# Optimization experiments

Hardware: AMD Instinct MI355X
Metric: run time of the kernel (lower is better)

Reference implementation:

```python
import jax, jax.numpy as jnp
import numpy as np

D = 1024
H = 16
DK = D // H


def setup_inputs() -> dict:
    key = jax.random.key(0)
    ks = jax.random.split(key, 10)
    B, S = 2, 2048
    scale = 1.0 / np.sqrt(D)
    inp = {
        "x": jax.random.normal(ks[0], (B, S, D), dtype=jnp.float32),
        "mask": jax.random.randint(ks[1], (B, S), 0, 2, dtype=jnp.int32),
        "wq": jax.random.normal(ks[2], (D, D), dtype=jnp.float32) * scale,
        "bq": jnp.zeros((D,), dtype=jnp.float32),
        "wk": jax.random.normal(ks[3], (D, D), dtype=jnp.float32) * scale,
        "bk": jnp.zeros((D,), dtype=jnp.float32),
        "wv": jax.random.normal(ks[4], (D, D), dtype=jnp.float32) * scale,
        "bv": jnp.zeros((D,), dtype=jnp.float32),
        "wo": jax.random.normal(ks[5], (D, D), dtype=jnp.float32) * scale,
        "bo": jnp.zeros((D,), dtype=jnp.float32),
    }
    return inp


def reference(x, mask, wq, bq, wk, bk, wv, bv, wo, bo):
    B, S, _ = x.shape
    # torch Linear: y = x @ W.T + b
    def proj(w, b):
        return (jnp.einsum("bsd,ed->bse", x, w) + b).reshape(B, S, H, DK).transpose(0, 2, 1, 3)  # (B,H,S,dk)

    q = proj(wq, bq)
    k = proj(wk, bk)
    v = proj(wv, bv)

    scores = jnp.einsum("bhqd,bhkd->bhqk", q, k) / jnp.sqrt(jnp.float32(DK))  # (B,H,S,S)
    # original: mask.unsqueeze(1).unsqueeze(3) -> (B,1,S,1), masks along the QUERY axis
    m = mask[:, None, :, None]  # (B,1,S,1)
    scores = jnp.where(m == 0, jnp.float32(-1e9), scores)
    attn = jax.nn.softmax(scores, axis=-1)
    ctx = jnp.einsum("bhqk,bhkd->bhqd", attn, v)  # (B,H,S,dk)
    concat = ctx.transpose(0, 2, 1, 3).reshape(B, S, D)
    return jnp.einsum("bsd,ed->bse", concat, wo) + bo
```

## Files before the change

### kernel.cpp

```cpp
#include <hip/hip_runtime.h>
#include <hip/hip_bf16.h>

#define SEQ 2048
#define DM  1024

typedef __attribute__((ext_vector_type(8))) _Float16 f16x8;
typedef __attribute__((ext_vector_type(4)))  float   f32x4;

#define EXP2F(x) __builtin_amdgcn_exp2f(x)

__device__ __forceinline__ ushort f2h(float x) {
    union { _Float16 h; ushort u; } c; c.h = (_Float16)x; return c.u;
}
__device__ __forceinline__ unsigned pk2h(float a, float b) {
    typedef __fp16 fp16v2 __attribute__((ext_vector_type(2)));
    union { fp16v2 h; unsigned u; } c;
    c.h = __builtin_amdgcn_cvt_pkrtz(a, b);
    return c.u;
}

__device__ __forceinline__ void gload16(const void* g, void* l) {
    __builtin_amdgcn_global_load_lds(
        (const __attribute__((address_space(1))) unsigned*)(uintptr_t)g,
        (__attribute__((address_space(3))) unsigned*)(uintptr_t)l, 16, 0, 0);
}

__global__ __launch_bounds__(256)
void cvt_all(const float* __restrict__ x,  const float* __restrict__ wq,
             const float* __restrict__ wk, const float* __restrict__ wv,
             const float* __restrict__ wo,
             ushort* __restrict__ xH, ushort* __restrict__ wH)
{
    const int NX4 = (2 * SEQ * DM) / 4;
    const int NW4 = (DM * DM) / 4;
    const int total = NX4 + 4 * NW4;
    for (int i = blockIdx.x * 256 + threadIdx.x; i < total; i += gridDim.x * 256) {
        float4 v; ushort4* dst;
        if (i < NX4) {
            v = ((const float4*)x)[i];
            dst = (ushort4*)xH + i;
        } else {
            const int j = i - NX4;
            const int wi = j >> 18;
            const int jo = j & (NW4 - 1);
            const float* ws_ = (wi == 0) ? wq : (wi == 1) ? wk : (wi == 2) ? wv : wo;
            v = ((const float4*)ws_)[jo];
            dst = (ushort4*)wH + j;
        }
        ushort4 h;
        h.x = f2h(v.x); h.y = f2h(v.y); h.z = f2h(v.z); h.w = f2h(v.w);
        *dst = h;
    }
}

template<int BM, int BN, int WM, int WN, int MODE>
__global__ __launch_bounds__(WM * WN * 64)
void gemm5(const ushort* __restrict__ A, const ushort* __restrict__ B,
           const float* __restrict__ b0, const float* __restrict__ b1,
           const float* __restrict__ b2,
           ushort* __restrict__ QH, ushort* __restrict__ KH,
           ushort* __restrict__ VH, float* __restrict__ outf, int nmt)
{
    constexpr int NW  = WM * WN;
    constexpr int PR  = BM / WM, PC = BN / WN;
    constexpr int MR  = PR / 16, NR = PC / 16, MH = MR / 2;
    constexpr int APW = (BM / 8) / NW;
    constexpr int BPW = (BN / 8) / NW;
    constexpr int NT  = DM / 64;

    __shared__ ushort A_lds[2][BM * 64];
    __shared__ ushort B_lds[2][BN * 64];

    const int tid = threadIdx.x, w = tid >> 6, lane = tid & 63;
    const int nwg = gridDim.x, q8 = nwg >> 3;
    const int wg  = (blockIdx.x & 7) * q8 + (blockIdx.x >> 3);
    const int m0  = (wg % nmt) * BM, n0 = (wg / nmt) * BN;
    const int wm  = w / WN, wn = w % WN;

    auto stage = [&](int buf, int kt) {
        const int k0 = kt * 64;
#pragma unroll
        for (int j = 0; j < APW; ++j) {
            const int s   = w * APW + j;
            const int row = s * 8 + (lane >> 3);
            const int cl  = (lane & 7) ^ (row & 7);
            gload16(A + (size_t)(m0 + row) * DM + k0 + cl * 8,
                    &A_lds[buf][s * 512]);
        }
#pragma unroll
        for (int j = 0; j < BPW; ++j) {
            const int s   = w * BPW + j;
            const int row = s * 8 + (lane >> 3);
            const int cl  = (lane & 7) ^ (row & 7);
            gload16(B + (size_t)(n0 + row) * DM + k0 + cl * 8,
                    &B_lds[buf][s * 512]);
        }
    };

    f32x4 acc[MR][NR];
#pragma unroll
    for (int i = 0; i < MR; ++i)
#pragma unroll
        for (int j = 0; j < NR; ++j) acc[i][j] = f32x4{0.f, 0.f, 0.f, 0.f};

    stage(0, 0);
    stage(1, 1);

    for (int t = 0; t < NT; ++t) {
        const int buf = t & 1;
        if (t == NT - 1) asm volatile("s_waitcnt vmcnt(0)" ::: "memory");
        else             asm volatile("s_waitcnt vmcnt(8)" ::: "memory");
        __builtin_amdgcn_sched_barrier(0);
        __builtin_amdgcn_s_barrier();

        f16x8 bf_[NR][2];
#pragma unroll
        for (int nf = 0; nf < NR; ++nf) {
            const int r = wn * PC + nf * 16 + (lane & 15);
#pragma unroll
            for (int kb = 0; kb < 2; ++kb) {
                const int c = kb * 4 + (lane >> 4);
                bf_[nf][kb] = *(const f16x8*)&B_lds[buf][r * 64 + ((c ^ (r & 7)) << 3)];
            }
        }
#pragma unroll
        for (int qm = 0; qm < 2; ++qm) {
            f16x8 af_[MH][2];
#pragma unroll
            for (int mf = 0; mf < MH; ++mf) {
                const int r = wm * PR + qm * (PR / 2) + mf * 16 + (lane & 15);
#pragma unroll
                for (int kb = 0; kb < 2; ++kb) {
                    const int c = kb * 4 + (lane >> 4);
                    af_[mf][kb] = *(const f16x8*)&A_lds[buf][r * 64 + ((c ^ (r & 7)) << 3)];
                }
            }
            __builtin_amdgcn_s_setprio(1);
#pragma unroll
            for (int kb = 0; kb < 2; ++kb)
#pragma unroll
                for (int mf = 0; mf < MH; ++mf)
#pragma unroll
                    for (int nf = 0; nf < NR; ++nf)
                        acc[qm * MH + mf][nf] = __builtin_amdgcn_mfma_f32_16x16x32_f16(
                            af_[mf][kb], bf_[nf][kb], acc[qm * MH + mf][nf], 0, 0, 0);
            __builtin_amdgcn_s_setprio(0);
        }
        __builtin_amdgcn_sched_barrier(0);
        __builtin_amdgcn_s_barrier();
        __builtin_amdgcn_sched_barrier(0);
        if (t + 2 < NT) stage(buf, t + 2);
    }

#pragma unroll
    for (int mf = 0; mf < MR; ++mf)
#pragma unroll
        for (int nf = 0; nf < NR; ++nf) {
            const int col  = n0 + wn * PC + nf * 16 + (lane & 15);
            const int row0 = m0 + wm * PR + mf * 16 + ((lane >> 4) << 2);
            f32x4 v = acc[mf][nf];
            if constexpr (MODE == 1) {
                float4 o;
                o.x = v[0] + b0[row0 + 0];
                o.y = v[1] + b0[row0 + 1];
                o.z = v[2] + b0[row0 + 2];
                o.w = v[3] + b0[row0 + 3];
                *(float4*)&outf[(size_t)col * DM + row0] = o;
            } else {
                const int sel = row0 >> 10;
                const int e = row0 & 1023;
                const int b = col >> 11, s = col & 2047;
                const int h = e >> 6, dk = e & 63;
                const float* bp = (sel == 0) ? b0 : (sel == 1) ? b1 : b2;
                const float sc = (sel == 0) ? 0.125f * 1.44269504089f : 1.0f;
                const float v0 = (v[0] + bp[e + 0]) * sc;
                const float v1 = (v[1] + bp[e + 1]) * sc;
                const float v2 = (v[2] + bp[e + 2]) * sc;
                const float v3 = (v[3] + bp[e + 3]) * sc;
                const int bh = b * 16 + h;
                ushort4 hv;
                hv.x = f2h(v0); hv.y = f2h(v1); hv.z = f2h(v2); hv.w = f2h(v3);
                if (sel == 0) {
                    const size_t off = ((size_t)bh * SEQ + s) * 64 + dk;
                    *(ushort4*)&QH[off] = hv;
                } else if (sel == 1) {
                    const size_t off = ((size_t)bh * SEQ + s) * 64 + dk;
                    *(ushort4*)&KH[off] = hv;
                } else {
                    const size_t o0 = ((size_t)bh * 64 + dk) * SEQ + s;
                    VH[o0]           = hv.x;
                    VH[o0 + SEQ]     = hv.y;
                    VH[o0 + 2 * SEQ] = hv.z;
                    VH[o0 + 3 * SEQ] = hv.w;
                }
            }
        }
}

__global__ __launch_bounds__(512, 2)
void attn_k(const ushort* __restrict__ QH, const ushort* __restrict__ KH,
            const ushort* __restrict__ VH, const int* __restrict__ mask,
            ushort* __restrict__ ch)
{
    __shared__ ushort Ks[2][64 * 64];
    __shared__ ushort Vs[2][64 * 64];
    __shared__ ushort Ps[8][16 * 64];

    const int t = threadIdx.x, w = t >> 6, lane = t & 63;
    const int wg = (blockIdx.x & 7) * 64 + (blockIdx.x >> 3);
    const int bh = wg >> 4, qt = wg & 15;
    const int b = bh >> 4, h = bh & 15;
    const int q0 = qt * 128 + w * 16;
    const size_t base = (size_t)bh * SEQ * 64;
    const int lq = lane & 15, cb = lane >> 4;

    const int msk = mask[b * SEQ + q0 + lq];
    f16x8 qf[2];
#pragma unroll
    for (int kb = 0; kb < 2; ++kb) {
        qf[kb] = *(const f16x8*)&QH[base + (size_t)(q0 + lq) * 64 + kb * 32 + cb * 8];
        if (msk == 0) qf[kb] = f16x8{0, 0, 0, 0, 0, 0, 0, 0};
    }

    float l_part = 0.f;
    f32x4 acc[4];
#pragma unroll
    for (int df = 0; df < 4; ++df) acc[df] = f32x4{0.f, 0.f, 0.f, 0.f};

    f16x8 sK, sV;
    const int sr = t >> 3, scc = t & 7;
    const int wr_off = sr * 64 + (scc ^ (sr & 7)) * 8;
    const ushort* gK = &KH[base + (size_t)sr * 64 + scc * 8];
    const ushort* gV = &VH[base + (size_t)sr * SEQ + scc * 8];
    auto stage_load = [&]() {
        sK = *(const f16x8*)gK;
        sV = *(const f16x8*)gV;
        gK += 4096;
        gV += 64;
    };

    stage_load();
    *(f16x8*)&Ks[0][wr_off] = sK;
    *(f16x8*)&Vs[0][wr_off] = sV;
    stage_load();
    __syncthreads();

    auto body = [&](const int BUF, const bool WR, const bool LD) {
        if (WR) {
            *(f16x8*)&Ks[BUF ^ 1][wr_off] = sK;
            *(f16x8*)&Vs[BUF ^ 1][wr_off] = sV;
        }
        if (LD) stage_load();

        f32x4 st[4];
#pragma unroll
        for (int mf = 0; mf < 4; ++mf) st[mf] = f32x4{0.f, 0.f, 0.f, 0.f};
        __builtin_amdgcn_s_setprio(1);
#pragma unroll
        for (int mf = 0; mf < 4; ++mf) {
            const int r = mf * 16 + lq;
#pragma unroll
            for (int kb = 0; kb < 2; ++kb) {
                const int p = (kb * 4 + cb) ^ (r & 7);
                f16x8 kf = *(const f16x8*)&Ks[BUF][r * 64 + p * 8];
                st[mf] = __builtin_amdgcn_mfma_f32_16x16x32_f16(kf, qf[kb], st[mf], 0, 0, 0);
            }
        }
        __builtin_amdgcn_s_setprio(0);

#pragma unroll
        for (int mf = 0; mf < 2; ++mf) {
            const float e0 = EXP2F(st[mf][0]);
            const float e1 = EXP2F(st[mf][1]);
            const float e2 = EXP2F(st[mf][2]);
            const float e3 = EXP2F(st[mf][3]);
            l_part += (e0 + e1) + (e2 + e3);
            uint2 pw;
            pw.x = pk2h(e0, e1);
            pw.y = pk2h(e2, e3);
            const int key0 = mf * 16 + (cb << 2);
            const int p = (key0 >> 3) ^ (lq & 7);
            *(uint2*)&Ps[w][lq * 64 + p * 8 + (key0 & 7)] = pw;
        }
        {
            const int p0 = cb ^ (lq & 7);
            f16x8 pf0 = *(const f16x8*)&Ps[w][lq * 64 + p0 * 8];
            __builtin_amdgcn_s_setprio(1);
#pragma unroll
            for (int df = 0; df < 4; ++df) {
                const int r = df * 16 + lq;
                const int p = cb ^ (r & 7);
                f16x8 vf = *(const f16x8*)&Vs[BUF][r * 64 + p * 8];
                acc[df] = __builtin_amdgcn_mfma_f32_16x16x32_f16(vf, pf0, acc[df], 0, 0, 0);
            }
            __builtin_amdgcn_s_setprio(0);
        }
#pragma unroll
        for (int mf = 2; mf < 4; ++mf) {
            const float e0 = EXP2F(st[mf][0]);
            const float e1 = EXP2F(st[mf][1]);
            const float e2 = EXP2F(st[mf][2]);
            const float e3 = EXP2F(st[mf][3]);
            l_part += (e0 + e1) + (e2 + e3);
            uint2 pw;
            pw.x = pk2h(e0, e1);
            pw.y = pk2h(e2, e3);
            const int key0 = mf * 16 + (cb << 2);
            const int p = (key0 >> 3) ^ (lq & 7);
            *(uint2*)&Ps[w][lq * 64 + p * 8 + (key0 & 7)] = pw;
        }
        {
            const int p1 = (4 + cb) ^ (lq & 7);
            f16x8 pf1 = *(const f16x8*)&Ps[w][lq * 64 + p1 * 8];
            __builtin_amdgcn_s_setprio(1);
#pragma unroll
            for (int df = 0; df < 4; ++df) {
                const int r = df * 16 + lq;
                const int p = (4 + cb) ^ (r & 7);
                f16x8 vf = *(const f16x8*)&Vs[BUF][r * 64 + p * 8];
                acc[df] = __builtin_amdgcn_mfma_f32_16x16x32_f16(vf, pf1, acc[df], 0, 0, 0);
            }
            __builtin_amdgcn_s_setprio(0);
        }

        __syncthreads();
    };

#pragma unroll 1
    for (int i = 0; i < 15; ++i) {
        body(0, true, true);
        body(1, true, true);
    }
    body(0, true, false);
    body(1, false, false);

    {
        float l_tot = l_part;
        l_tot += __shfl_xor(l_tot, 16);
        l_tot += __shfl_xor(l_tot, 32);
        const float inv = 1.0f / l_tot;
        const int s = q0 + lq;
#pragma unroll
        for (int df = 0; df < 4; ++df) {
            const int e0 = h * 64 + df * 16 + (cb << 2);
            ushort4 hv;
            hv.x = f2h(acc[df][0] * inv);
            hv.y = f2h(acc[df][1] * inv);
            hv.z = f2h(acc[df][2] * inv);
            hv.w = f2h(acc[df][3] * inv);
            *(ushort4*)&ch[(size_t)(b * SEQ + s) * DM + e0] = hv;
        }
    }
}

extern "C" void kernel_launch(void* const* d_in, const int* in_sizes, int n_in,
                              void* d_out, int out_size, void* d_ws, size_t ws_size,
                              hipStream_t stream)
{
    const float* x  = (const float*)d_in[0];
    const int* mask = (const int*)d_in[1];
    const float* wq = (const float*)d_in[2];
    const float* bq = (const float*)d_in[3];
    const float* wk = (const float*)d_in[4];
    const float* bk = (const float*)d_in[5];
    const float* wv = (const float*)d_in[6];
    const float* bv = (const float*)d_in[7];
    const float* wo = (const float*)d_in[8];
    const float* bo = (const float*)d_in[9];
    float* out = (float*)d_out;

    const size_t M1 = 1024 * 1024;
    ushort* W = (ushort*)d_ws;
    ushort* xH = W;
    ushort* wH = W + 4 * M1;
    ushort* QH = W + 8 * M1;
    ushort* KH = W + 12 * M1;
    ushort* VH = W + 16 * M1;

    cvt_all<<<2048, 256, 0, stream>>>(x, wq, wk, wv, wo, xH, wH);

    gemm5<384, 128, 4, 2, 0><<<256, 512, 0, stream>>>(
        wH, xH, bq, bk, bv, QH, KH, VH, nullptr, 8);

    attn_k<<<512, 512, 0, stream>>>(QH, KH, VH, mask, xH);

    gemm5<128, 128, 2, 2, 1><<<256, 256, 0, stream>>>(
        wH + 3 * M1, xH, bo, nullptr, nullptr,
        nullptr, nullptr, nullptr, out, 8);
}
```

Measured before the change: 104.1 us.

## Process two K/V tiles per barrier with four-slot LDS ring

Measured after the change: 104.3 us. No clear change (+0.2%).

```diff
diff --git a/kernel.cpp b/kernel.cpp
--- a/kernel.cpp
+++ b/kernel.cpp
@@ -202,8 +202,8 @@
             const ushort* __restrict__ VH, const int* __restrict__ mask,
             ushort* __restrict__ ch)
 {
-    __shared__ ushort Ks[2][64 * 64];
-    __shared__ ushort Vs[2][64 * 64];
+    __shared__ ushort Ks[4][64 * 64];
+    __shared__ ushort Vs[4][64 * 64];
     __shared__ ushort Ps[8][16 * 64];
 
     const int t = threadIdx.x, w = t >> 6, lane = t & 63;
@@ -227,31 +227,25 @@
 #pragma unroll
     for (int df = 0; df < 4; ++df) acc[df] = f32x4{0.f, 0.f, 0.f, 0.f};
 
-    f16x8 sK, sV;
+    f16x8 sK0, sV0, sK1, sV1;
     const int sr = t >> 3, scc = t & 7;
     const int wr_off = sr * 64 + (scc ^ (sr & 7)) * 8;
     const ushort* gK = &KH[base + (size_t)sr * 64 + scc * 8];
     const ushort* gV = &VH[base + (size_t)sr * SEQ + scc * 8];
-    auto stage_load = [&]() {
-        sK = *(const f16x8*)gK;
-        sV = *(const f16x8*)gV;
-        gK += 4096;
-        gV += 64;
+    auto load_pair = [&]() {
+        sK0 = *(const f16x8*)gK; gK += 4096;
+        sV0 = *(const f16x8*)gV; gV += 64;
+        sK1 = *(const f16x8*)gK; gK += 4096;
+        sV1 = *(const f16x8*)gV; gV += 64;
     };
 
-    stage_load();
-    *(f16x8*)&Ks[0][wr_off] = sK;
-    *(f16x8*)&Vs[0][wr_off] = sV;
-    stage_load();
+    load_pair();
+    *(f16x8*)&Ks[0][wr_off] = sK0;  *(f16x8*)&Vs[0][wr_off] = sV0;
+    *(f16x8*)&Ks[1][wr_off] = sK1;  *(f16x8*)&Vs[1][wr_off] = sV1;
+    load_pair();
     __syncthreads();
 
-    auto body = [&](const int BUF, const bool WR, const bool LD) {
-        if (WR) {
-            *(f16x8*)&Ks[BUF ^ 1][wr_off] = sK;
-            *(f16x8*)&Vs[BUF ^ 1][wr_off] = sV;
-        }
-        if (LD) stage_load();
-
+    auto compute = [&](const int BUF) {
         f32x4 st[4];
 #pragma unroll
         for (int mf = 0; mf < 4; ++mf) st[mf] = f32x4{0.f, 0.f, 0.f, 0.f};
@@ -322,17 +316,30 @@
             }
             __builtin_amdgcn_s_setprio(0);
         }
-
-        __syncthreads();
     };
 
+    auto step = [&](const int PH, const bool WR, const bool LD) {
+        if (WR) {
+            const int w0 = PH ? 0 : 2, w1 = PH ? 1 : 3;
+            *(f16x8*)&Ks[w0][wr_off] = sK0;  *(f16x8*)&Vs[w0][wr_off] = sV0;
+            *(f16x8*)&Ks[w1][wr_off] = sK1;  *(f16x8*)&Vs[w1][wr_off] = sV1;
+        }
+        if (LD) load_pair();
+        compute(PH ? 2 : 0);
+        compute(PH ? 3 : 1);
+        __builtin_amdgcn_sched_barrier(0);
+        asm volatile("s_waitcnt lgkmcnt(0)" ::: "memory");
+        __builtin_amdgcn_s_barrier();
+        __builtin_amdgcn_sched_barrier(0);
+    };
+
 #pragma unroll 1
-    for (int i = 0; i < 15; ++i) {
-        body(0, true, true);
-        body(1, true, true);
-    }
-    body(0, true, false);
-    body(1, false, false);
+    for (int i = 0; i < 7; ++i) {
+        step(0, true, true);
+        step(1, true, true);
+    }
+    step(0, true, false);
+    step(1, false, false);
 
     {
         float l_tot = l_part;
```

## Load K/V fragments directly from global memory, dropping LDS staging and block barriers

Applied to the files above, without the earlier changes.

Result: slower. 285.2 us (+173.9%).

```diff
diff --git a/kernel.cpp b/kernel.cpp
--- a/kernel.cpp
+++ b/kernel.cpp
@@ -197,20 +197,18 @@
         }
 }
 
-__global__ __launch_bounds__(512, 2)
+__global__ __launch_bounds__(256, 4)
 void attn_k(const ushort* __restrict__ QH, const ushort* __restrict__ KH,
             const ushort* __restrict__ VH, const int* __restrict__ mask,
             ushort* __restrict__ ch)
 {
-    __shared__ ushort Ks[2][64 * 64];
-    __shared__ ushort Vs[2][64 * 64];
-    __shared__ ushort Ps[8][16 * 64];
+    __shared__ ushort Ps[4][16 * 64];
 
     const int t = threadIdx.x, w = t >> 6, lane = t & 63;
-    const int wg = (blockIdx.x & 7) * 64 + (blockIdx.x >> 3);
-    const int bh = wg >> 4, qt = wg & 15;
+    const int wg = (blockIdx.x & 7) * 128 + (blockIdx.x >> 3);
+    const int bh = wg >> 5, qt = wg & 31;
     const int b = bh >> 4, h = bh & 15;
-    const int q0 = qt * 128 + w * 16;
+    const int q0 = qt * 64 + w * 16;
     const size_t base = (size_t)bh * SEQ * 64;
     const int lq = lane & 15, cb = lane >> 4;
 
@@ -227,45 +225,36 @@
 #pragma unroll
     for (int df = 0; df < 4; ++df) acc[df] = f32x4{0.f, 0.f, 0.f, 0.f};
 
-    f16x8 sK, sV;
-    const int sr = t >> 3, scc = t & 7;
-    const int wr_off = sr * 64 + (scc ^ (sr & 7)) * 8;
-    const ushort* gK = &KH[base + (size_t)sr * 64 + scc * 8];
-    const ushort* gV = &VH[base + (size_t)sr * SEQ + scc * 8];
-    auto stage_load = [&]() {
-        sK = *(const f16x8*)gK;
-        sV = *(const f16x8*)gV;
-        gK += 4096;
-        gV += 64;
-    };
-
-    stage_load();
-    *(f16x8*)&Ks[0][wr_off] = sK;
-    *(f16x8*)&Vs[0][wr_off] = sV;
-    stage_load();
-    __syncthreads();
-
-    auto body = [&](const int BUF, const bool WR, const bool LD) {
-        if (WR) {
-            *(f16x8*)&Ks[BUF ^ 1][wr_off] = sK;
-            *(f16x8*)&Vs[BUF ^ 1][wr_off] = sV;
-        }
-        if (LD) stage_load();
+    const ushort* Kp = KH + base + (size_t)lq * 64 + cb * 8;
+    const ushort* Vp = VH + base + (size_t)lq * SEQ + cb * 8;
+
+#pragma unroll 1
+    for (int kt = 0; kt < SEQ / 64; ++kt) {
+        const int k64 = kt * 64;
+
+        f16x8 kf[4][2];
+#pragma unroll
+        for (int mf = 0; mf < 4; ++mf)
+#pragma unroll
+            for (int kb = 0; kb < 2; ++kb)
+                kf[mf][kb] = *(const f16x8*)&Kp[(size_t)(k64 + mf * 16) * 64 + kb * 32];
+
+        f16x8 vf[4][2];
+#pragma unroll
+        for (int df = 0; df < 4; ++df)
+#pragma unroll
+            for (int kb = 0; kb < 2; ++kb)
+                vf[df][kb] = *(const f16x8*)&Vp[(size_t)df * 16 * SEQ + k64 + kb * 32];
 
         f32x4 st[4];
 #pragma unroll
         for (int mf = 0; mf < 4; ++mf) st[mf] = f32x4{0.f, 0.f, 0.f, 0.f};
         __builtin_amdgcn_s_setprio(1);
 #pragma unroll
-        for (int mf = 0; mf < 4; ++mf) {
-            const int r = mf * 16 + lq;
-#pragma unroll
-            for (int kb = 0; kb < 2; ++kb) {
-                const int p = (kb * 4 + cb) ^ (r & 7);
-                f16x8 kf = *(const f16x8*)&Ks[BUF][r * 64 + p * 8];
-                st[mf] = __builtin_amdgcn_mfma_f32_16x16x32_f16(kf, qf[kb], st[mf], 0, 0, 0);
-            }
-        }
+        for (int mf = 0; mf < 4; ++mf)
+#pragma unroll
+            for (int kb = 0; kb < 2; ++kb)
+                st[mf] = __builtin_amdgcn_mfma_f32_16x16x32_f16(kf[mf][kb], qf[kb], st[mf], 0, 0, 0);
         __builtin_amdgcn_s_setprio(0);
 
 #pragma unroll
@@ -287,12 +276,8 @@
             f16x8 pf0 = *(const f16x8*)&Ps[w][lq * 64 + p0 * 8];
             __builtin_amdgcn_s_setprio(1);
 #pragma unroll
-            for (int df = 0; df < 4; ++df) {
-                const int r = df * 16 + lq;
-                const int p = cb ^ (r & 7);
-                f16x8 vf = *(const f16x8*)&Vs[BUF][r * 64 + p * 8];
-                acc[df] = __builtin_amdgcn_mfma_f32_16x16x32_f16(vf, pf0, acc[df], 0, 0, 0);
-            }
+            for (int df = 0; df < 4; ++df)
+                acc[df] = __builtin_amdgcn_mfma_f32_16x16x32_f16(vf[df][0], pf0, acc[df], 0, 0, 0);
             __builtin_amdgcn_s_setprio(0);
         }
 #pragma unroll
@@ -314,25 +299,11 @@
             f16x8 pf1 = *(const f16x8*)&Ps[w][lq * 64 + p1 * 8];
             __builtin_amdgcn_s_setprio(1);
 #pragma unroll
-            for (int df = 0; df < 4; ++df) {
-                const int r = df * 16 + lq;
-                const int p = (4 + cb) ^ (r & 7);
-                f16x8 vf = *(const f16x8*)&Vs[BUF][r * 64 + p * 8];
-                acc[df] = __builtin_amdgcn_mfma_f32_16x16x32_f16(vf, pf1, acc[df], 0, 0, 0);
-            }
+            for (int df = 0; df < 4; ++df)
+                acc[df] = __builtin_amdgcn_mfma_f32_16x16x32_f16(vf[df][1], pf1, acc[df], 0, 0, 0);
             __builtin_amdgcn_s_setprio(0);
         }
-
-        __syncthreads();
-    };
-
-#pragma unroll 1
-    for (int i = 0; i < 15; ++i) {
-        body(0, true, true);
-        body(1, true, true);
-    }
-    body(0, true, false);
-    body(1, false, false);
+    }
 
     {
         float l_tot = l_part;
@@ -382,7 +353,7 @@
     gemm5<384, 128, 4, 2, 0><<<256, 512, 0, stream>>>(
         wH, xH, bq, bk, bv, QH, KH, VH, nullptr, 8);
 
-    attn_k<<<512, 512, 0, stream>>>(QH, KH, VH, mask, xH);
+    attn_k<<<1024, 256, 0, stream>>>(QH, KH, VH, mask, xH);
 
     gemm5<128, 128, 2, 2, 1><<<256, 256, 0, stream>>>(
         wH + 3 * M1, xH, bo, nullptr, nullptr,
```
